# Performance work log

Measured on AMD Instinct MI355X. Metric: run time of the kernel, lower is better.

Reference implementation:

```python
import jax, jax.numpy as jnp
import numpy as np

LN_EPS = 1e-5

def _layernorm(x, g, b):
    mu = jnp.mean(x, axis=-1, keepdims=True)
    var = jnp.var(x, axis=-1, keepdims=True)
    return (x - mu) * jax.lax.rsqrt(var + LN_EPS) * g + b

def setup_inputs() -> dict:
    key = jax.random.key(0)
    ks = jax.random.split(key, 12)
    B, E, R = 32, 64, 36
    Dt, Di, D = 768, 2048, 512
    s = 0.02
    return {
        "text_feats": jax.random.normal(ks[0], (B, E, Dt), jnp.float32),
        "image_feats": jax.random.normal(ks[1], (B, R, Di), jnp.float32),
        "W_text": jax.random.normal(ks[2], (Dt, D), jnp.float32) * s,
        "b_text": jnp.zeros((D,), jnp.float32),
        "g_text": jnp.ones((D,), jnp.float32),
        "beta_text": jnp.zeros((D,), jnp.float32),
        "W_img": jax.random.normal(ks[3], (Di, D), jnp.float32) * s,
        "b_img": jnp.zeros((D,), jnp.float32),
        "g_img": jnp.ones((D,), jnp.float32),
        "beta_img": jnp.zeros((D,), jnp.float32),
        "W1": jax.random.normal(ks[4], (2 * D, D), jnp.float32) * s,
        "b1": jnp.zeros((D,), jnp.float32),
        "W2": jax.random.normal(ks[5], (D, 1), jnp.float32) * s,
        "b2": jnp.zeros((1,), jnp.float32),
    }

def reference(text_feats, image_feats, W_text, b_text, g_text, beta_text,
              W_img, b_img, g_img, beta_img, W1, b1, W2, b2):
    B, E, _ = text_feats.shape
    R = image_feats.shape[1]
    D = W_text.shape[1]
    # projections: Linear -> ReLU -> LayerNorm
    text_aligned = _layernorm(jax.nn.relu(text_feats @ W_text + b_text), g_text, beta_text)   # [B,E,D]
    image_aligned = _layernorm(jax.nn.relu(image_feats @ W_img + b_img), g_img, beta_img)     # [B,R,D]
    # pairwise scorer: split W1 to avoid materializing the [B,E,R,2D] concat
    W1_t, W1_i = W1[:D], W1[D:]
    h_t = text_aligned @ W1_t                 # [B,E,D]
    h_i = image_aligned @ W1_i + b1           # [B,R,D]
    h = jax.nn.relu(h_t[:, :, None, :] + h_i[:, None, :, :])  # [B,E,R,D]
    scores_raw = jnp.squeeze(h @ W2, -1) + b2[0]               # [B,E,R]
    alignment_scores = jax.nn.sigmoid(scores_raw)
    # softmax over flattened (E*R) per batch
    w = jax.nn.softmax(alignment_scores.reshape(B, E * R), axis=1).reshape(B, E, R)
    # weighted sum over regions, mean over entities
    aggregated = jnp.einsum('ber,brd->bd', w, image_aligned) / E   # [B,D]
    return alignment_scores, aggregated
```

## Files before the change

kernel.cpp:

```cpp
#include <hip/hip_runtime.h>
#include <math.h>

#define LN_EPS 1e-5f

typedef __attribute__((ext_vector_type(8))) short bf16x8;
typedef __attribute__((ext_vector_type(4))) float f32x4;
typedef unsigned short ushort_t;
typedef unsigned int uint_t;

__device__ __forceinline__ ushort_t f2bf(float f) {
    uint_t u = __float_as_uint(f);
    u += 0x7FFF + ((u >> 16) & 1);
    return (ushort_t)(u >> 16);
}

__global__ __launch_bounds__(256) void prep_kernel(
    const float* __restrict__ text, const float* __restrict__ image,
    ushort_t* __restrict__ text_bf, ushort_t* __restrict__ image_bf,
    const float* __restrict__ W_text, const float* __restrict__ W_img,
    const float* __restrict__ W1,
    ushort_t* __restrict__ Wt_t, ushort_t* __restrict__ Wi_t,
    ushort_t* __restrict__ W1t_t, ushort_t* __restrict__ W1i_t)
{
    __shared__ float t[32][33];
    const int bid = blockIdx.x;
    if (bid < 3840) {
        const int i4 = (bid * 256 + threadIdx.x) * 4;
        const float* src; ushort_t* dst; int off;
        if (i4 < 1572864) { src = text;  dst = text_bf;  off = i4; }
        else              { src = image; dst = image_bf; off = i4 - 1572864; }
        float4 v = *(const float4*)(src + off);
        ushort4 o;
        o.x = f2bf(v.x); o.y = f2bf(v.y); o.z = f2bf(v.z); o.w = f2bf(v.w);
        *(ushort4*)(dst + off) = o;
        return;
    }
    int local = bid - 3840;
    const float* src; ushort_t* dst; int K;
    if      (local < 384)  { src = W_text;         dst = Wt_t;  K = 768;  }
    else if (local < 1408) { src = W_img;          dst = Wi_t;  K = 2048; local -= 384; }
    else if (local < 1664) { src = W1;             dst = W1t_t; K = 512;  local -= 1408; }
    else                   { src = W1 + 512 * 512; dst = W1i_t; K = 512;  local -= 1664; }
    const int ntk = K / 32;
    const int k0 = (local % ntk) * 32;
    const int n0 = (local / ntk) * 32;
    const int x = threadIdx.x % 32, y = threadIdx.x / 32;
    #pragma unroll
    for (int j = 0; j < 4; ++j)
        t[y + 8 * j][x] = src[(size_t)(k0 + y + 8 * j) * 512 + n0 + x];
    __syncthreads();
    #pragma unroll
    for (int j = 0; j < 4; ++j)
        dst[(size_t)(n0 + y + 8 * j) * K + k0 + x] = f2bf(t[x][y + 8 * j]);
}

__global__ __launch_bounds__(256) void gemm_splitk_kernel(
    const ushort_t* __restrict__ A0, const ushort_t* __restrict__ B0,
    const float* __restrict__ bias0, float* __restrict__ C0, int K0,
    const ushort_t* __restrict__ A1, const ushort_t* __restrict__ B1,
    const float* __restrict__ bias1, float* __restrict__ C1, int K1,
    int ysplit, int relu)
{
    __shared__ float red[4][64][64];

    const ushort_t* A; const ushort_t* Bt; const float* bias; float* C; int K;
    int yy = blockIdx.y;
    if (yy < ysplit) { A = A0; Bt = B0; bias = bias0; C = C0; K = K0; }
    else { A = A1; Bt = B1; bias = bias1; C = C1; K = K1; yy -= ysplit; }

    const int tid  = threadIdx.x;
    const int wave = tid >> 6;
    const int lane = tid & 63;
    const int q    = lane >> 4;
    const int mj   = lane & 15;
    const int brow = yy * 64;
    const int bcol = blockIdx.x * 64;

    const ushort_t* Ab = A  + (size_t)(brow + mj) * K + q * 8;
    const ushort_t* Bb = Bt + (size_t)(bcol + mj) * K + q * 8;
    const int kw0    = wave * (K >> 2);
    const int ksteps = K >> 7;

    f32x4 acc[4][4] = {};

    #pragma unroll 2
    for (int s = 0; s < ksteps; ++s) {
        const int k = kw0 + s * 32;
        bf16x8 af[4], bf[4];
        #pragma unroll
        for (int i = 0; i < 4; ++i) {
            af[i] = *(const bf16x8*)(Ab + (size_t)i * 16 * K + k);
            bf[i] = *(const bf16x8*)(Bb + (size_t)i * 16 * K + k);
        }
        #pragma unroll
        for (int mi = 0; mi < 4; ++mi)
            #pragma unroll
            for (int ni = 0; ni < 4; ++ni)
                acc[mi][ni] = __builtin_amdgcn_mfma_f32_16x16x32_bf16(
                    af[mi], bf[ni], acc[mi][ni], 0, 0, 0);
    }

    #pragma unroll
    for (int mi = 0; mi < 4; ++mi)
        #pragma unroll
        for (int ni = 0; ni < 4; ++ni)
            #pragma unroll
            for (int r = 0; r < 4; ++r)
                red[wave][mi * 16 + q * 4 + r][ni * 16 + mj] = acc[mi][ni][r];
    __syncthreads();

    #pragma unroll
    for (int g = 0; g < 4; ++g) {
        const int idx = g * 1024 + tid * 4;
        const int row = idx >> 6, col = idx & 63;
        float4 v0 = *(float4*)&red[0][row][col];
        float4 v1 = *(float4*)&red[1][row][col];
        float4 v2 = *(float4*)&red[2][row][col];
        float4 v3 = *(float4*)&red[3][row][col];
        float4 o;
        o.x = (v0.x + v1.x) + (v2.x + v3.x);
        o.y = (v0.y + v1.y) + (v2.y + v3.y);
        o.z = (v0.z + v1.z) + (v2.z + v3.z);
        o.w = (v0.w + v1.w) + (v2.w + v3.w);
        if (bias) {
            float4 bv = *(const float4*)&bias[bcol + col];
            o.x += bv.x; o.y += bv.y; o.z += bv.z; o.w += bv.w;
        }
        if (relu) {
            o.x = fmaxf(o.x, 0.f); o.y = fmaxf(o.y, 0.f);
            o.z = fmaxf(o.z, 0.f); o.w = fmaxf(o.w, 0.f);
        }
        *(float4*)&C[(size_t)(brow + row) * 512 + bcol + col] = o;
    }
}

__global__ __launch_bounds__(256) void ln_fused_kernel(
    float* __restrict__ ta, const float* __restrict__ g_t,
    const float* __restrict__ be_t, ushort_t* __restrict__ ta_bf,
    float* __restrict__ ia, const float* __restrict__ g_i,
    const float* __restrict__ be_i, ushort_t* __restrict__ ia_bf)
{
    const int tid = threadIdx.x;
    int row = blockIdx.x;
    float* p; const float* g; const float* beta; ushort_t* obf; float* ofp;
    if (row < 2048) {
        p = ta + (size_t)row * 512; g = g_t; beta = be_t;
        obf = ta_bf + (size_t)row * 512; ofp = nullptr;
    } else {
        row -= 2048;
        p = ia + (size_t)row * 512; g = g_i; beta = be_i;
        obf = ia_bf + (size_t)row * 512; ofp = p;
    }

    float2 v = *(const float2*)&p[tid * 2];
    float s  = v.x + v.y;
    float ss = v.x * v.x + v.y * v.y;
    #pragma unroll
    for (int off = 32; off; off >>= 1) {
        s  += __shfl_down(s, off);
        ss += __shfl_down(ss, off);
    }
    __shared__ float red[8];
    if ((tid & 63) == 0) { red[(tid >> 6) * 2] = s; red[(tid >> 6) * 2 + 1] = ss; }
    __syncthreads();
    __shared__ float stats[2];
    if (tid == 0) {
        float S  = red[0] + red[2] + red[4] + red[6];
        float SS = red[1] + red[3] + red[5] + red[7];
        float mu  = S * (1.f / 512.f);
        float var = SS * (1.f / 512.f) - mu * mu;
        stats[0] = mu;
        stats[1] = rsqrtf(var + LN_EPS);
    }
    __syncthreads();
    const float mu = stats[0], rstd = stats[1];
    float2 gv = *(const float2*)&g[tid * 2];
    float2 bv = *(const float2*)&beta[tid * 2];
    float o0 = (v.x - mu) * rstd * gv.x + bv.x;
    float o1 = (v.y - mu) * rstd * gv.y + bv.y;
    ushort2 ob; ob.x = f2bf(o0); ob.y = f2bf(o1);
    *(ushort2*)&obf[tid * 2] = ob;
    if (ofp) {
        float2 of; of.x = o0; of.y = o1;
        *(float2*)&ofp[tid * 2] = of;
    }
}

__global__ __launch_bounds__(256) void scores_kernel(
    const float* __restrict__ ht, const float* __restrict__ hi,
    const float* __restrict__ W2, const float* __restrict__ b2,
    float* __restrict__ scores)
{
    const int be   = blockIdx.x;
    const int b    = be >> 6;
    const int tid  = threadIdx.x;
    const int lane = tid & 63;
    const int wave = tid >> 6;

    float htv[8], w2v[8];
    const float* htp = ht + (size_t)be * 512;
    #pragma unroll
    for (int j = 0; j < 8; ++j) {
        htv[j] = htp[lane + 64 * j];
        w2v[j] = W2[lane + 64 * j];
    }
    const float bb = b2[0];
    const float* hib = hi + (size_t)b * 36 * 512;

    for (int r = wave; r < 36; r += 4) {
        const float* hir = hib + (size_t)r * 512;
        float acc = 0.f;
        #pragma unroll
        for (int j = 0; j < 8; ++j) {
            float h = fmaxf(htv[j] + hir[lane + 64 * j], 0.f);
            acc = fmaf(h, w2v[j], acc);
        }
        #pragma unroll
        for (int off = 32; off; off >>= 1) acc += __shfl_down(acc, off);
        if (lane == 0) {
            float sr = acc + bb;
            scores[(size_t)be * 36 + r] = 1.f / (1.f + expf(-sr));
        }
    }
}

__global__ __launch_bounds__(256) void agg_kernel(
    const float* __restrict__ scores, const float* __restrict__ img,
    float* __restrict__ outAgg)
{
    const int b   = blockIdx.x;
    const int tid = threadIdx.x;
    const float* sc = scores + (size_t)b * 2304;

    __shared__ float part[4][36];
    __shared__ float sexp[36];
    __shared__ float inv_s;

    const int e4 = tid >> 6;
    const int r  = tid & 63;
    if (r < 36) {
        float p = 0.f;
        #pragma unroll
        for (int e = 0; e < 16; ++e) p += expf(sc[(e * 4 + e4) * 36 + r]);
        part[e4][r] = p;
    }
    __syncthreads();
    if (tid < 36) sexp[tid] = part[0][tid] + part[1][tid] + part[2][tid] + part[3][tid];
    __syncthreads();
    if (tid < 64) {
        float v = (tid < 36) ? sexp[tid] : 0.f;
        #pragma unroll
        for (int off = 32; off; off >>= 1) v += __shfl_down(v, off);
        if (tid == 0) inv_s = 1.f / (v * 64.f);
    }
    __syncthreads();
    const float inv = inv_s;

    const float* ib = img + (size_t)b * 36 * 512;
    for (int d = tid; d < 512; d += 256) {
        float acc = 0.f;
        #pragma unroll
        for (int rr = 0; rr < 36; ++rr)
            acc = fmaf(sexp[rr] * inv, ib[rr * 512 + d], acc);
        outAgg[(size_t)b * 512 + d] = acc;
    }
}

extern "C" void kernel_launch(void* const* d_in, const int* in_sizes, int n_in,
                              void* d_out, int out_size, void* d_ws, size_t ws_size,
                              hipStream_t stream)
{
    const float* text      = (const float*)d_in[0];
    const float* image     = (const float*)d_in[1];
    const float* W_text    = (const float*)d_in[2];
    const float* b_text    = (const float*)d_in[3];
    const float* g_text    = (const float*)d_in[4];
    const float* beta_text = (const float*)d_in[5];
    const float* W_img     = (const float*)d_in[6];
    const float* b_img     = (const float*)d_in[7];
    const float* g_img     = (const float*)d_in[8];
    const float* beta_img  = (const float*)d_in[9];
    const float* W1        = (const float*)d_in[10];
    const float* b1        = (const float*)d_in[11];
    const float* W2        = (const float*)d_in[12];
    const float* b2        = (const float*)d_in[13];

    float* out_scores = (float*)d_out;
    float* out_agg    = (float*)d_out + 73728;

    char* ws = (char*)d_ws;
    float*    ta       = (float*)(ws);
    float*    ia       = (float*)(ws + (4u << 20));
    ushort_t* text_bf  = (ushort_t*)(ws + 6402048);
    ushort_t* image_bf = (ushort_t*)(ws + 6402048 + 3145728);
    float*    ht       = (float*)(ws + 6402048);
    float*    hi       = (float*)(ws + 6402048 + 4194304);
    char*     wbase    = ws + 6402048 + 7864320;
    ushort_t* Wt_t     = (ushort_t*)(wbase);
    ushort_t* Wi_t     = (ushort_t*)(wbase + 786432);
    ushort_t* W1t_t    = (ushort_t*)(wbase + 786432 + 2097152);
    ushort_t* W1i_t    = (ushort_t*)(wbase + 786432 + 2097152 + 524288);
    char*     bfbase   = wbase + 786432 + 2097152 + 2 * 524288;
    ushort_t* ta_bf    = (ushort_t*)(bfbase);
    ushort_t* ia_bf    = (ushort_t*)(bfbase + 2097152);

    prep_kernel<<<5760, 256, 0, stream>>>(text, image, text_bf, image_bf,
                                          W_text, W_img, W1,
                                          Wt_t, Wi_t, W1t_t, W1i_t);
    gemm_splitk_kernel<<<dim3(8, 50), 256, 0, stream>>>(
        text_bf, Wt_t, b_text, ta, 768,
        image_bf, Wi_t, b_img, ia, 2048,
        32, 1);
    ln_fused_kernel<<<3200, 256, 0, stream>>>(ta, g_text, beta_text, ta_bf,
                                              ia, g_img, beta_img, ia_bf);
    gemm_splitk_kernel<<<dim3(8, 50), 256, 0, stream>>>(
        ta_bf, W1t_t, nullptr, ht, 512,
        ia_bf, W1i_t, b1, hi, 512,
        32, 0);
    scores_kernel<<<2048, 256, 0, stream>>>(ht, hi, W2, b2, out_scores);
    agg_kernel<<<32, 256, 0, stream>>>(out_scores, ia, out_agg);
}
```

Baseline: 150.2 us.

## Fuse all stages into one persistent kernel with software grid barriers

Replaces six kernel launches with a single persistent kernel of 1024 blocks that runs prep, projection GEMM, layernorm, second GEMM, scoring and aggregation. Stages are separated by hierarchical atomic grid barriers, which removes launch gaps and inter-kernel drain. It also changes the GEMM wave split from 4-way split-K to 2 K-halves by 2 N-halves, halving the reduction buffer, and splits aggregation across 64 blocks. The risks are barrier overhead, a deadlock if the 1024 blocks cannot all be resident at once, idle blocks during the 400-tile GEMM phases, and an extra memset launch.

```diff
diff --git a/kernel.cpp b/kernel.cpp
--- a/kernel.cpp
+++ b/kernel.cpp
@@ -2,6 +2,7 @@
 #include <math.h>
 
 #define LN_EPS 1e-5f
+#define NBLK 1024
 
 typedef __attribute__((ext_vector_type(8))) short bf16x8;
 typedef __attribute__((ext_vector_type(4))) float f32x4;
@@ -14,88 +15,66 @@
     return (ushort_t)(u >> 16);
 }
 
-__global__ __launch_bounds__(256) void prep_kernel(
-    const float* __restrict__ text, const float* __restrict__ image,
-    ushort_t* __restrict__ text_bf, ushort_t* __restrict__ image_bf,
-    const float* __restrict__ W_text, const float* __restrict__ W_img,
-    const float* __restrict__ W1,
-    ushort_t* __restrict__ Wt_t, ushort_t* __restrict__ Wi_t,
-    ushort_t* __restrict__ W1t_t, ushort_t* __restrict__ W1i_t)
+union SMU {
+    float red[2][64][64];
+    float tmat[32][33];
+    struct { float red8[8]; float stats[2]; } ln;
+    struct { float part[4][36]; float sexp[36]; float inv_s; } agg;
+};
+
+__device__ __forceinline__ void gbar(uint_t* cnt, int phase) {
+    __syncthreads();
+    if (threadIdx.x == 0) {
+        __threadfence();
+        uint_t* sub = cnt + (blockIdx.x & 15) * 32;
+        uint_t* mst = cnt + 512;
+        uint_t old = atomicAdd(sub, 1u);
+        if (old == (uint_t)(phase * (NBLK / 16) - 1))
+            atomicAdd(mst, 1u);
+        int it = 0;
+        while (__hip_atomic_load(mst, __ATOMIC_RELAXED, __HIP_MEMORY_SCOPE_AGENT)
+               < (uint_t)(phase * 16)) {
+            __builtin_amdgcn_s_sleep(4);
+            if (++it > (1 << 20)) break;
+        }
+        __threadfence();
+    }
+    __syncthreads();
+}
+
+__device__ __forceinline__ void do_gemm(
+    const ushort_t* __restrict__ A, const ushort_t* __restrict__ Bt,
+    const float* __restrict__ bias, float* __restrict__ C, int K,
+    int yy, int bx, int relu, float (&red)[2][64][64])
 {
-    __shared__ float t[32][33];
-    const int bid = blockIdx.x;
-    if (bid < 3840) {
-        const int i4 = (bid * 256 + threadIdx.x) * 4;
-        const float* src; ushort_t* dst; int off;
-        if (i4 < 1572864) { src = text;  dst = text_bf;  off = i4; }
-        else              { src = image; dst = image_bf; off = i4 - 1572864; }
-        float4 v = *(const float4*)(src + off);
-        ushort4 o;
-        o.x = f2bf(v.x); o.y = f2bf(v.y); o.z = f2bf(v.z); o.w = f2bf(v.w);
-        *(ushort4*)(dst + off) = o;
-        return;
-    }
-    int local = bid - 3840;
-    const float* src; ushort_t* dst; int K;
-    if      (local < 384)  { src = W_text;         dst = Wt_t;  K = 768;  }
-    else if (local < 1408) { src = W_img;          dst = Wi_t;  K = 2048; local -= 384; }
-    else if (local < 1664) { src = W1;             dst = W1t_t; K = 512;  local -= 1408; }
-    else                   { src = W1 + 512 * 512; dst = W1i_t; K = 512;  local -= 1664; }
-    const int ntk = K / 32;
-    const int k0 = (local % ntk) * 32;
-    const int n0 = (local / ntk) * 32;
-    const int x = threadIdx.x % 32, y = threadIdx.x / 32;
-    #pragma unroll
-    for (int j = 0; j < 4; ++j)
-        t[y + 8 * j][x] = src[(size_t)(k0 + y + 8 * j) * 512 + n0 + x];
-    __syncthreads();
-    #pragma unroll
-    for (int j = 0; j < 4; ++j)
-        dst[(size_t)(n0 + y + 8 * j) * K + k0 + x] = f2bf(t[x][y + 8 * j]);
-}
-
-__global__ __launch_bounds__(256) void gemm_splitk_kernel(
-    const ushort_t* __restrict__ A0, const ushort_t* __restrict__ B0,
-    const float* __restrict__ bias0, float* __restrict__ C0, int K0,
-    const ushort_t* __restrict__ A1, const ushort_t* __restrict__ B1,
-    const float* __restrict__ bias1, float* __restrict__ C1, int K1,
-    int ysplit, int relu)
-{
-    __shared__ float red[4][64][64];
-
-    const ushort_t* A; const ushort_t* Bt; const float* bias; float* C; int K;
-    int yy = blockIdx.y;
-    if (yy < ysplit) { A = A0; Bt = B0; bias = bias0; C = C0; K = K0; }
-    else { A = A1; Bt = B1; bias = bias1; C = C1; K = K1; yy -= ysplit; }
-
     const int tid  = threadIdx.x;
     const int wave = tid >> 6;
     const int lane = tid & 63;
+    const int kw   = wave >> 1;
+    const int nw   = wave & 1;
     const int q    = lane >> 4;
     const int mj   = lane & 15;
     const int brow = yy * 64;
-    const int bcol = blockIdx.x * 64;
-
-    const ushort_t* Ab = A  + (size_t)(brow + mj) * K + q * 8;
-    const ushort_t* Bb = Bt + (size_t)(bcol + mj) * K + q * 8;
-    const int kw0    = wave * (K >> 2);
-    const int ksteps = K >> 7;
-
-    f32x4 acc[4][4] = {};
-
+    const int bcol = bx * 64;
+
+    const ushort_t* Ab = A  + (size_t)(brow + mj) * K + kw * (K >> 1) + q * 8;
+    const ushort_t* Bb = Bt + (size_t)(bcol + nw * 32 + mj) * K + kw * (K >> 1) + q * 8;
+    const int ksteps = K >> 6;
+
+    f32x4 acc[4][2] = {};
     #pragma unroll 2
     for (int s = 0; s < ksteps; ++s) {
-        const int k = kw0 + s * 32;
-        bf16x8 af[4], bf[4];
-        #pragma unroll
-        for (int i = 0; i < 4; ++i) {
-            af[i] = *(const bf16x8*)(Ab + (size_t)i * 16 * K + k);
-            bf[i] = *(const bf16x8*)(Bb + (size_t)i * 16 * K + k);
-        }
+        bf16x8 af[4], bf[2];
+        #pragma unroll
+        for (int i = 0; i < 4; ++i)
+            af[i] = *(const bf16x8*)(Ab + (size_t)i * 16 * K + s * 32);
+        #pragma unroll
+        for (int i = 0; i < 2; ++i)
+            bf[i] = *(const bf16x8*)(Bb + (size_t)i * 16 * K + s * 32);
         #pragma unroll
         for (int mi = 0; mi < 4; ++mi)
             #pragma unroll
-            for (int ni = 0; ni < 4; ++ni)
+            for (int ni = 0; ni < 2; ++ni)
                 acc[mi][ni] = __builtin_amdgcn_mfma_f32_16x16x32_bf16(
                     af[mi], bf[ni], acc[mi][ni], 0, 0, 0);
     }
@@ -103,10 +82,10 @@
     #pragma unroll
     for (int mi = 0; mi < 4; ++mi)
         #pragma unroll
-        for (int ni = 0; ni < 4; ++ni)
+        for (int ni = 0; ni < 2; ++ni)
             #pragma unroll
             for (int r = 0; r < 4; ++r)
-                red[wave][mi * 16 + q * 4 + r][ni * 16 + mj] = acc[mi][ni][r];
+                red[kw][mi * 16 + q * 4 + r][nw * 32 + ni * 16 + mj] = acc[mi][ni][r];
     __syncthreads();
 
     #pragma unroll
@@ -115,13 +94,9 @@
         const int row = idx >> 6, col = idx & 63;
         float4 v0 = *(float4*)&red[0][row][col];
         float4 v1 = *(float4*)&red[1][row][col];
-        float4 v2 = *(float4*)&red[2][row][col];
-        float4 v3 = *(float4*)&red[3][row][col];
         float4 o;
-        o.x = (v0.x + v1.x) + (v2.x + v3.x);
-        o.y = (v0.y + v1.y) + (v2.y + v3.y);
-        o.z = (v0.z + v1.z) + (v2.z + v3.z);
-        o.w = (v0.w + v1.w) + (v2.w + v3.w);
+        o.x = v0.x + v1.x; o.y = v0.y + v1.y;
+        o.z = v0.z + v1.z; o.w = v0.w + v1.w;
         if (bias) {
             float4 bv = *(const float4*)&bias[bcol + col];
             o.x += bv.x; o.y += bv.y; o.z += bv.z; o.w += bv.w;
@@ -134,135 +109,186 @@
     }
 }
 
-__global__ __launch_bounds__(256) void ln_fused_kernel(
-    float* __restrict__ ta, const float* __restrict__ g_t,
-    const float* __restrict__ be_t, ushort_t* __restrict__ ta_bf,
-    float* __restrict__ ia, const float* __restrict__ g_i,
-    const float* __restrict__ be_i, ushort_t* __restrict__ ia_bf)
+__global__ __launch_bounds__(256, 4) void mega_kernel(
+    const float* __restrict__ text, const float* __restrict__ image,
+    const float* __restrict__ W_text, const float* __restrict__ b_text,
+    const float* __restrict__ g_text, const float* __restrict__ beta_text,
+    const float* __restrict__ W_img, const float* __restrict__ b_img,
+    const float* __restrict__ g_img, const float* __restrict__ beta_img,
+    const float* __restrict__ W1, const float* __restrict__ b1,
+    const float* __restrict__ W2, const float* __restrict__ b2,
+    float* __restrict__ out_scores, float* __restrict__ out_agg,
+    float* ta, float* ia, ushort_t* text_bf, ushort_t* image_bf,
+    float* ht, float* hi,
+    ushort_t* Wt_t, ushort_t* Wi_t, ushort_t* W1t_t, ushort_t* W1i_t,
+    ushort_t* ta_bf, ushort_t* ia_bf, uint_t* cnt)
 {
+    __shared__ SMU sm;
     const int tid = threadIdx.x;
-    int row = blockIdx.x;
-    float* p; const float* g; const float* beta; ushort_t* obf; float* ofp;
-    if (row < 2048) {
-        p = ta + (size_t)row * 512; g = g_t; beta = be_t;
-        obf = ta_bf + (size_t)row * 512; ofp = nullptr;
-    } else {
-        row -= 2048;
-        p = ia + (size_t)row * 512; g = g_i; beta = be_i;
-        obf = ia_bf + (size_t)row * 512; ofp = p;
-    }
-
-    float2 v = *(const float2*)&p[tid * 2];
-    float s  = v.x + v.y;
-    float ss = v.x * v.x + v.y * v.y;
-    #pragma unroll
-    for (int off = 32; off; off >>= 1) {
-        s  += __shfl_down(s, off);
-        ss += __shfl_down(ss, off);
-    }
-    __shared__ float red[8];
-    if ((tid & 63) == 0) { red[(tid >> 6) * 2] = s; red[(tid >> 6) * 2 + 1] = ss; }
-    __syncthreads();
-    __shared__ float stats[2];
-    if (tid == 0) {
-        float S  = red[0] + red[2] + red[4] + red[6];
-        float SS = red[1] + red[3] + red[5] + red[7];
-        float mu  = S * (1.f / 512.f);
-        float var = SS * (1.f / 512.f) - mu * mu;
-        stats[0] = mu;
-        stats[1] = rsqrtf(var + LN_EPS);
-    }
-    __syncthreads();
-    const float mu = stats[0], rstd = stats[1];
-    float2 gv = *(const float2*)&g[tid * 2];
-    float2 bv = *(const float2*)&beta[tid * 2];
-    float o0 = (v.x - mu) * rstd * gv.x + bv.x;
-    float o1 = (v.y - mu) * rstd * gv.y + bv.y;
-    ushort2 ob; ob.x = f2bf(o0); ob.y = f2bf(o1);
-    *(ushort2*)&obf[tid * 2] = ob;
-    if (ofp) {
-        float2 of; of.x = o0; of.y = o1;
-        *(float2*)&ofp[tid * 2] = of;
-    }
-}
-
-__global__ __launch_bounds__(256) void scores_kernel(
-    const float* __restrict__ ht, const float* __restrict__ hi,
-    const float* __restrict__ W2, const float* __restrict__ b2,
-    float* __restrict__ scores)
-{
-    const int be   = blockIdx.x;
-    const int b    = be >> 6;
-    const int tid  = threadIdx.x;
-    const int lane = tid & 63;
-    const int wave = tid >> 6;
-
-    float htv[8], w2v[8];
-    const float* htp = ht + (size_t)be * 512;
-    #pragma unroll
-    for (int j = 0; j < 8; ++j) {
-        htv[j] = htp[lane + 64 * j];
-        w2v[j] = W2[lane + 64 * j];
-    }
-    const float bb = b2[0];
-    const float* hib = hi + (size_t)b * 36 * 512;
-
-    for (int r = wave; r < 36; r += 4) {
-        const float* hir = hib + (size_t)r * 512;
+    const int bid = blockIdx.x;
+
+    for (int vb = bid; vb < 5760; vb += NBLK) {
+        if (vb < 3840) {
+            const int i4 = (vb * 256 + tid) * 4;
+            const float* src; ushort_t* dst; int off;
+            if (i4 < 1572864) { src = text;  dst = text_bf;  off = i4; }
+            else              { src = image; dst = image_bf; off = i4 - 1572864; }
+            float4 v = *(const float4*)(src + off);
+            ushort4 o;
+            o.x = f2bf(v.x); o.y = f2bf(v.y); o.z = f2bf(v.z); o.w = f2bf(v.w);
+            *(ushort4*)(dst + off) = o;
+        } else {
+            int local = vb - 3840;
+            const float* src; ushort_t* dst; int K;
+            if      (local < 384)  { src = W_text;       dst = Wt_t;  K = 768;  }
+            else if (local < 1408) { src = W_img;        dst = Wi_t;  K = 2048; local -= 384; }
+            else if (local < 1664) { src = W1;           dst = W1t_t; K = 512;  local -= 1408; }
+            else                   { src = W1 + 512*512; dst = W1i_t; K = 512;  local -= 1664; }
+            const int ntk = K / 32;
+            const int k0 = (local % ntk) * 32;
+            const int n0 = (local / ntk) * 32;
+            const int x = tid % 32, y = tid / 32;
+            #pragma unroll
+            for (int j = 0; j < 4; ++j)
+                sm.tmat[y + 8 * j][x] = src[(size_t)(k0 + y + 8 * j) * 512 + n0 + x];
+            __syncthreads();
+            #pragma unroll
+            for (int j = 0; j < 4; ++j)
+                dst[(size_t)(n0 + y + 8 * j) * K + k0 + x] = f2bf(sm.tmat[x][y + 8 * j]);
+            __syncthreads();
+        }
+    }
+    gbar(cnt, 1);
+
+    if (bid < 400) {
+        const int t  = (bid & 7) * 50 + (bid >> 3);
+        const int yy = t >> 3, x = t & 7;
+        if (yy < 32) do_gemm(text_bf,  Wt_t, b_text, ta, 768,  yy,      x, 1, sm.red);
+        else         do_gemm(image_bf, Wi_t, b_img,  ia, 2048, yy - 32, x, 1, sm.red);
+    }
+    gbar(cnt, 2);
+
+    for (int rr = bid; rr < 3200; rr += NBLK) {
+        int row = rr;
+        float* p; const float* g; const float* beta; ushort_t* obf; float* ofp;
+        if (row < 2048) {
+            p = ta + (size_t)row * 512; g = g_text; beta = beta_text;
+            obf = ta_bf + (size_t)row * 512; ofp = nullptr;
+        } else {
+            row -= 2048;
+            p = ia + (size_t)row * 512; g = g_img; beta = beta_img;
+            obf = ia_bf + (size_t)row * 512; ofp = ia + (size_t)row * 512;
+        }
+        float2 v = *(const float2*)&p[tid * 2];
+        float s  = v.x + v.y;
+        float ss = v.x * v.x + v.y * v.y;
+        #pragma unroll
+        for (int off = 32; off; off >>= 1) {
+            s  += __shfl_down(s, off);
+            ss += __shfl_down(ss, off);
+        }
+        if ((tid & 63) == 0) {
+            sm.ln.red8[(tid >> 6) * 2]     = s;
+            sm.ln.red8[(tid >> 6) * 2 + 1] = ss;
+        }
+        __syncthreads();
+        if (tid == 0) {
+            float S  = sm.ln.red8[0] + sm.ln.red8[2] + sm.ln.red8[4] + sm.ln.red8[6];
+            float SS = sm.ln.red8[1] + sm.ln.red8[3] + sm.ln.red8[5] + sm.ln.red8[7];
+            float mu  = S * (1.f / 512.f);
+            float var = SS * (1.f / 512.f) - mu * mu;
+            sm.ln.stats[0] = mu;
+            sm.ln.stats[1] = rsqrtf(var + LN_EPS);
+        }
+        __syncthreads();
+        const float mu = sm.ln.stats[0], rstd = sm.ln.stats[1];
+        float2 gv = *(const float2*)&g[tid * 2];
+        float2 bv = *(const float2*)&beta[tid * 2];
+        float o0 = (v.x - mu) * rstd * gv.x + bv.x;
+        float o1 = (v.y - mu) * rstd * gv.y + bv.y;
+        ushort2 ob; ob.x = f2bf(o0); ob.y = f2bf(o1);
+        *(ushort2*)&obf[tid * 2] = ob;
+        if (ofp) { float2 of; of.x = o0; of.y = o1; *(float2*)&ofp[tid * 2] = of; }
+        __syncthreads();
+    }
+    gbar(cnt, 3);
+
+    if (bid < 400) {
+        const int t  = (bid & 7) * 50 + (bid >> 3);
+        const int yy = t >> 3, x = t & 7;
+        if (yy < 32) do_gemm(ta_bf, W1t_t, nullptr, ht, 512, yy,      x, 0, sm.red);
+        else         do_gemm(ia_bf, W1i_t, b1,      hi, 512, yy - 32, x, 0, sm.red);
+    }
+    gbar(cnt, 4);
+
+    {
+        const int lane = tid & 63;
+        const int wave = tid >> 6;
+        float w2v[8];
+        #pragma unroll
+        for (int j = 0; j < 8; ++j) w2v[j] = W2[lane + 64 * j];
+        const float bb = b2[0];
+        const int sbe = ((bid & 7) << 7) + (bid >> 3);
+        #pragma unroll
+        for (int u = 0; u < 2; ++u) {
+            const int be = sbe + u * 1024;
+            const int b  = be >> 6;
+            float htv[8];
+            const float* htp = ht + (size_t)be * 512;
+            #pragma unroll
+            for (int j = 0; j < 8; ++j) htv[j] = htp[lane + 64 * j];
+            const float* hib = hi + (size_t)b * 36 * 512;
+            for (int r = wave; r < 36; r += 4) {
+                const float* hir = hib + (size_t)r * 512;
+                float acc = 0.f;
+                #pragma unroll
+                for (int j = 0; j < 8; ++j) {
+                    float h = fmaxf(htv[j] + hir[lane + 64 * j], 0.f);
+                    acc = fmaf(h, w2v[j], acc);
+                }
+                #pragma unroll
+                for (int off = 32; off; off >>= 1) acc += __shfl_down(acc, off);
+                if (lane == 0) {
+                    float sr = acc + bb;
+                    out_scores[(size_t)be * 36 + r] = 1.f / (1.f + expf(-sr));
+                }
+            }
+        }
+    }
+    gbar(cnt, 5);
+
+    if (bid < 64) {
+        const int b  = bid >> 1;
+        const int d0 = (bid & 1) << 8;
+        const float* sc = out_scores + (size_t)b * 2304;
+        const int e4 = tid >> 6;
+        const int r  = tid & 63;
+        if (r < 36) {
+            float p = 0.f;
+            #pragma unroll
+            for (int e = 0; e < 16; ++e) p += expf(sc[(e * 4 + e4) * 36 + r]);
+            sm.agg.part[e4][r] = p;
+        }
+        __syncthreads();
+        if (tid < 36)
+            sm.agg.sexp[tid] = sm.agg.part[0][tid] + sm.agg.part[1][tid]
+                             + sm.agg.part[2][tid] + sm.agg.part[3][tid];
+        __syncthreads();
+        if (tid < 64) {
+            float v = (tid < 36) ? sm.agg.sexp[tid] : 0.f;
+            #pragma unroll
+            for (int off = 32; off; off >>= 1) v += __shfl_down(v, off);
+            if (tid == 0) sm.agg.inv_s = 1.f / (v * 64.f);
+        }
+        __syncthreads();
+        const float inv = sm.agg.inv_s;
+        const float* ib = ia + (size_t)b * 36 * 512;
+        const int d = d0 + tid;
         float acc = 0.f;
         #pragma unroll
-        for (int j = 0; j < 8; ++j) {
-            float h = fmaxf(htv[j] + hir[lane + 64 * j], 0.f);
-            acc = fmaf(h, w2v[j], acc);
-        }
-        #pragma unroll
-        for (int off = 32; off; off >>= 1) acc += __shfl_down(acc, off);
-        if (lane == 0) {
-            float sr = acc + bb;
-            scores[(size_t)be * 36 + r] = 1.f / (1.f + expf(-sr));
-        }
-    }
-}
-
-__global__ __launch_bounds__(256) void agg_kernel(
-    const float* __restrict__ scores, const float* __restrict__ img,
-    float* __restrict__ outAgg)
-{
-    const int b   = blockIdx.x;
-    const int tid = threadIdx.x;
-    const float* sc = scores + (size_t)b * 2304;
-
-    __shared__ float part[4][36];
-    __shared__ float sexp[36];
-    __shared__ float inv_s;
-
-    const int e4 = tid >> 6;
-    const int r  = tid & 63;
-    if (r < 36) {
-        float p = 0.f;
-        #pragma unroll
-        for (int e = 0; e < 16; ++e) p += expf(sc[(e * 4 + e4) * 36 + r]);
-        part[e4][r] = p;
-    }
-    __syncthreads();
-    if (tid < 36) sexp[tid] = part[0][tid] + part[1][tid] + part[2][tid] + part[3][tid];
-    __syncthreads();
-    if (tid < 64) {
-        float v = (tid < 36) ? sexp[tid] : 0.f;
-        #pragma unroll
-        for (int off = 32; off; off >>= 1) v += __shfl_down(v, off);
-        if (tid == 0) inv_s = 1.f / (v * 64.f);
-    }
-    __syncthreads();
-    const float inv = inv_s;
-
-    const float* ib = img + (size_t)b * 36 * 512;
-    for (int d = tid; d < 512; d += 256) {
-        float acc = 0.f;
-        #pragma unroll
-        for (int rr = 0; rr < 36; ++rr)
-            acc = fmaf(sexp[rr] * inv, ib[rr * 512 + d], acc);
-        outAgg[(size_t)b * 512 + d] = acc;
+        for (int rr2 = 0; rr2 < 36; ++rr2)
+            acc = fmaf(sm.agg.sexp[rr2] * inv, ib[rr2 * 512 + d], acc);
+        out_agg[(size_t)b * 512 + d] = acc;
     }
 }
 
@@ -303,20 +329,13 @@
     char*     bfbase   = wbase + 786432 + 2097152 + 2 * 524288;
     ushort_t* ta_bf    = (ushort_t*)(bfbase);
     ushort_t* ia_bf    = (ushort_t*)(bfbase + 2097152);
-
-    prep_kernel<<<5760, 256, 0, stream>>>(text, image, text_bf, image_bf,
-                                          W_text, W_img, W1,
-                                          Wt_t, Wi_t, W1t_t, W1i_t);
-    gemm_splitk_kernel<<<dim3(8, 50), 256, 0, stream>>>(
-        text_bf, Wt_t, b_text, ta, 768,
-        image_bf, Wi_t, b_img, ia, 2048,
-        32, 1);
-    ln_fused_kernel<<<3200, 256, 0, stream>>>(ta, g_text, beta_text, ta_bf,
-                                              ia, g_img, beta_img, ia_bf);
-    gemm_splitk_kernel<<<dim3(8, 50), 256, 0, stream>>>(
-        ta_bf, W1t_t, nullptr, ht, 512,
-        ia_bf, W1i_t, b1, hi, 512,
-        32, 0);
-    scores_kernel<<<2048, 256, 0, stream>>>(ht, hi, W2, b2, out_scores);
-    agg_kernel<<<32, 256, 0, stream>>>(out_scores, ia, out_agg);
-}
+    uint_t*   cnt      = (uint_t*)(ws + 25165824);
+
+    (void)hipMemsetAsync(cnt, 0, 4096, stream);
+    mega_kernel<<<NBLK, 256, 0, stream>>>(
+        text, image, W_text, b_text, g_text, beta_text,
+        W_img, b_img, g_img, beta_img, W1, b1, W2, b2,
+        out_scores, out_agg,
+        ta, ia, text_bf, image_bf, ht, hi,
+        Wt_t, Wi_t, W1t_t, W1i_t, ta_bf, ia_bf, cnt);
+}
```

Result: slower. 367.5 us (+144.6%).

## Fold LayerNorm into GEMM epilogues via atomic row stats and folded weights

Applied to the files above, without the earlier changes.

Removes the standalone LayerNorm kernel. The first GEMM's epilogue emits bf16 pre-norm activations and accumulates per-row sum and sum-of-squares with atomics. The second GEMM applies mean and rstd algebraically, using gamma folded into W1 and precomputed gamma·W1 and beta·W1 vectors. The aggregation kernel likewise applies normalization through coefficients, which saves a kernel launch and a full read/write pass over the activations. In exchange it adds atomics, a stats-zeroing block in prep, and extra bf16 rounding on the un-normalized activations, which may cost accuracy.

```diff
diff --git a/kernel.cpp b/kernel.cpp
--- a/kernel.cpp
+++ b/kernel.cpp
@@ -19,13 +19,17 @@
     ushort_t* __restrict__ text_bf, ushort_t* __restrict__ image_bf,
     const float* __restrict__ W_text, const float* __restrict__ W_img,
     const float* __restrict__ W1,
+    const float* __restrict__ g_text, const float* __restrict__ beta_text,
+    const float* __restrict__ g_img, const float* __restrict__ beta_img,
     ushort_t* __restrict__ Wt_t, ushort_t* __restrict__ Wi_t,
-    ushort_t* __restrict__ W1t_t, ushort_t* __restrict__ W1i_t)
+    ushort_t* __restrict__ W1t_g, ushort_t* __restrict__ W1i_g,
+    float* __restrict__ stats, float* __restrict__ vparts)
 {
     __shared__ float t[32][33];
     const int bid = blockIdx.x;
+    const int tid = threadIdx.x;
     if (bid < 3840) {
-        const int i4 = (bid * 256 + threadIdx.x) * 4;
+        const int i4 = (bid * 256 + tid) * 4;
         const float* src; ushort_t* dst; int off;
         if (i4 < 1572864) { src = text;  dst = text_bf;  off = i4; }
         else              { src = image; dst = image_bf; off = i4 - 1572864; }
@@ -36,53 +40,67 @@
         return;
     }
     int local = bid - 3840;
-    const float* src; ushort_t* dst; int K;
-    if      (local < 384)  { src = W_text;         dst = Wt_t;  K = 768;  }
-    else if (local < 1408) { src = W_img;          dst = Wi_t;  K = 2048; local -= 384; }
-    else if (local < 1664) { src = W1;             dst = W1t_t; K = 512;  local -= 1408; }
-    else                   { src = W1 + 512 * 512; dst = W1i_t; K = 512;  local -= 1664; }
-    const int ntk = K / 32;
-    const int k0 = (local % ntk) * 32;
-    const int n0 = (local / ntk) * 32;
-    const int x = threadIdx.x % 32, y = threadIdx.x / 32;
-    #pragma unroll
-    for (int j = 0; j < 4; ++j)
-        t[y + 8 * j][x] = src[(size_t)(k0 + y + 8 * j) * 512 + n0 + x];
-    __syncthreads();
-    #pragma unroll
-    for (int j = 0; j < 4; ++j)
-        dst[(size_t)(n0 + y + 8 * j) * K + k0 + x] = f2bf(t[x][y + 8 * j]);
-}
-
-__global__ __launch_bounds__(256) void gemm_splitk_kernel(
-    const ushort_t* __restrict__ A0, const ushort_t* __restrict__ B0,
-    const float* __restrict__ bias0, float* __restrict__ C0, int K0,
-    const ushort_t* __restrict__ A1, const ushort_t* __restrict__ B1,
-    const float* __restrict__ bias1, float* __restrict__ C1, int K1,
-    int ysplit, int relu)
-{
-    __shared__ float red[4][64][64];
-
-    const ushort_t* A; const ushort_t* Bt; const float* bias; float* C; int K;
-    int yy = blockIdx.y;
-    if (yy < ysplit) { A = A0; Bt = B0; bias = bias0; C = C0; K = K0; }
-    else { A = A1; Bt = B1; bias = bias1; C = C1; K = K1; yy -= ysplit; }
-
-    const int tid  = threadIdx.x;
-    const int wave = tid >> 6;
-    const int lane = tid & 63;
-    const int q    = lane >> 4;
-    const int mj   = lane & 15;
-    const int brow = yy * 64;
-    const int bcol = blockIdx.x * 64;
-
+    if (local < 1920) {
+        const float* src; ushort_t* dst; int K; const float* gs = nullptr;
+        if      (local < 384)  { src = W_text;       dst = Wt_t;  K = 768;  }
+        else if (local < 1408) { src = W_img;        dst = Wi_t;  K = 2048; local -= 384; }
+        else if (local < 1664) { src = W1;           dst = W1t_g; K = 512;  local -= 1408; gs = g_text; }
+        else                   { src = W1 + 512*512; dst = W1i_g; K = 512;  local -= 1664; gs = g_img; }
+        const int ntk = K / 32;
+        const int k0 = (local % ntk) * 32;
+        const int n0 = (local / ntk) * 32;
+        const int x = tid % 32, y = tid / 32;
+        #pragma unroll
+        for (int j = 0; j < 4; ++j)
+            t[y + 8 * j][x] = src[(size_t)(k0 + y + 8 * j) * 512 + n0 + x];
+        __syncthreads();
+        const float gv = gs ? gs[k0 + x] : 1.f;
+        #pragma unroll
+        for (int j = 0; j < 4; ++j)
+            dst[(size_t)(n0 + y + 8 * j) * K + k0 + x] = f2bf(t[x][y + 8 * j] * gv);
+        return;
+    }
+    if (local == 1920) {
+        for (int i = tid; i < 6400; i += 256) stats[i] = 0.f;
+        return;
+    }
+    {
+        const int j    = local - 1921;
+        const int half = j >> 2;
+        const int jj   = j & 3;
+        const float* cg = half ? g_img : g_text;
+        const float* cb = half ? beta_img : beta_text;
+        const float* Wb = W1 + (size_t)(half * 512 + jj * 128) * 512;
+        const int n = tid;
+        float ag0 = 0.f, ab0 = 0.f, ag1 = 0.f, ab1 = 0.f;
+        #pragma unroll 4
+        for (int k = 0; k < 128; ++k) {
+            const float c1 = cg[jj * 128 + k];
+            const float c2 = cb[jj * 128 + k];
+            const float w0 = Wb[(size_t)k * 512 + n];
+            const float w1 = Wb[(size_t)k * 512 + n + 256];
+            ag0 = fmaf(c1, w0, ag0); ab0 = fmaf(c2, w0, ab0);
+            ag1 = fmaf(c1, w1, ag1); ab1 = fmaf(c2, w1, ab1);
+        }
+        float* vg = vparts + (size_t)(half * 2 + 0) * 2048 + jj * 512;
+        float* vb = vparts + (size_t)(half * 2 + 1) * 2048 + jj * 512;
+        vg[n] = ag0; vg[n + 256] = ag1;
+        vb[n] = ab0; vb[n + 256] = ab1;
+    }
+}
+
+__device__ __forceinline__ void gemm_core(
+    const ushort_t* __restrict__ A, const ushort_t* __restrict__ Bt, int K,
+    int brow, int bcol, int wave, int lane, float (&red)[4][64][64])
+{
+    const int q  = lane >> 4;
+    const int mj = lane & 15;
     const ushort_t* Ab = A  + (size_t)(brow + mj) * K + q * 8;
     const ushort_t* Bb = Bt + (size_t)(bcol + mj) * K + q * 8;
     const int kw0    = wave * (K >> 2);
     const int ksteps = K >> 7;
 
     f32x4 acc[4][4] = {};
-
     #pragma unroll 2
     for (int s = 0; s < ksteps; ++s) {
         const int k = kw0 + s * 32;
@@ -99,7 +117,6 @@
                 acc[mi][ni] = __builtin_amdgcn_mfma_f32_16x16x32_bf16(
                     af[mi], bf[ni], acc[mi][ni], 0, 0, 0);
     }
-
     #pragma unroll
     for (int mi = 0; mi < 4; ++mi)
         #pragma unroll
@@ -108,6 +125,28 @@
             for (int r = 0; r < 4; ++r)
                 red[wave][mi * 16 + q * 4 + r][ni * 16 + mj] = acc[mi][ni][r];
     __syncthreads();
+}
+
+__global__ __launch_bounds__(256) void gemm1_kernel(
+    const ushort_t* __restrict__ A0, const ushort_t* __restrict__ B0,
+    const float* __restrict__ bias0, ushort_t* __restrict__ Cb0,
+    float* __restrict__ Cf0, float* __restrict__ st0, int K0,
+    const ushort_t* __restrict__ A1, const ushort_t* __restrict__ B1,
+    const float* __restrict__ bias1, ushort_t* __restrict__ Cb1,
+    float* __restrict__ Cf1, float* __restrict__ st1, int K1,
+    int ysplit)
+{
+    __shared__ float red[4][64][64];
+    const ushort_t* A; const ushort_t* Bt; const float* bias;
+    ushort_t* Cb; float* Cf; float* st; int K;
+    int yy = blockIdx.y;
+    if (yy < ysplit) { A=A0; Bt=B0; bias=bias0; Cb=Cb0; Cf=Cf0; st=st0; K=K0; }
+    else { A=A1; Bt=B1; bias=bias1; Cb=Cb1; Cf=Cf1; st=st1; K=K1; yy -= ysplit; }
+
+    const int tid  = threadIdx.x;
+    const int brow = yy * 64;
+    const int bcol = blockIdx.x * 64;
+    gemm_core(A, Bt, K, brow, bcol, tid >> 6, tid & 63, red);
 
     #pragma unroll
     for (int g = 0; g < 4; ++g) {
@@ -122,67 +161,89 @@
         o.y = (v0.y + v1.y) + (v2.y + v3.y);
         o.z = (v0.z + v1.z) + (v2.z + v3.z);
         o.w = (v0.w + v1.w) + (v2.w + v3.w);
+        float4 bv = *(const float4*)&bias[bcol + col];
+        o.x = fmaxf(o.x + bv.x, 0.f); o.y = fmaxf(o.y + bv.y, 0.f);
+        o.z = fmaxf(o.z + bv.z, 0.f); o.w = fmaxf(o.w + bv.w, 0.f);
+        ushort4 ob;
+        ob.x = f2bf(o.x); ob.y = f2bf(o.y); ob.z = f2bf(o.z); ob.w = f2bf(o.w);
+        *(ushort4*)&Cb[(size_t)(brow + row) * 512 + bcol + col] = ob;
+        if (Cf) *(float4*)&Cf[(size_t)(brow + row) * 512 + bcol + col] = o;
+        float s1 = (o.x + o.y) + (o.z + o.w);
+        float s2 = fmaf(o.x, o.x, fmaf(o.y, o.y, fmaf(o.z, o.z, o.w * o.w)));
+        #pragma unroll
+        for (int off = 8; off; off >>= 1) {
+            s1 += __shfl_down(s1, off, 16);
+            s2 += __shfl_down(s2, off, 16);
+        }
+        if ((tid & 15) == 0) {
+            atomicAdd(&st[(size_t)(brow + row) * 2],     s1);
+            atomicAdd(&st[(size_t)(brow + row) * 2 + 1], s2);
+        }
+    }
+}
+
+__global__ __launch_bounds__(256) void gemm2_kernel(
+    const ushort_t* __restrict__ A0, const ushort_t* __restrict__ B0,
+    const float* __restrict__ bias0, float* __restrict__ C0,
+    const float* __restrict__ st0, const float* __restrict__ gW0,
+    const float* __restrict__ bW0, int K0,
+    const ushort_t* __restrict__ A1, const ushort_t* __restrict__ B1,
+    const float* __restrict__ bias1, float* __restrict__ C1,
+    const float* __restrict__ st1, const float* __restrict__ gW1,
+    const float* __restrict__ bW1, int K1,
+    int ysplit)
+{
+    __shared__ float red[4][64][64];
+    const ushort_t* A; const ushort_t* Bt; const float* bias; float* C;
+    const float* st; const float* gW; const float* bW; int K;
+    int yy = blockIdx.y;
+    if (yy < ysplit) { A=A0; Bt=B0; bias=bias0; C=C0; st=st0; gW=gW0; bW=bW0; K=K0; }
+    else { A=A1; Bt=B1; bias=bias1; C=C1; st=st1; gW=gW1; bW=bW1; K=K1; yy -= ysplit; }
+
+    const int tid  = threadIdx.x;
+    const int brow = yy * 64;
+    const int bcol = blockIdx.x * 64;
+    gemm_core(A, Bt, K, brow, bcol, tid >> 6, tid & 63, red);
+
+    #pragma unroll
+    for (int g = 0; g < 4; ++g) {
+        const int idx = g * 1024 + tid * 4;
+        const int row = idx >> 6, col = idx & 63;
+        float4 v0 = *(float4*)&red[0][row][col];
+        float4 v1 = *(float4*)&red[1][row][col];
+        float4 v2 = *(float4*)&red[2][row][col];
+        float4 v3 = *(float4*)&red[3][row][col];
+        float4 s;
+        s.x = (v0.x + v1.x) + (v2.x + v3.x);
+        s.y = (v0.y + v1.y) + (v2.y + v3.y);
+        s.z = (v0.z + v1.z) + (v2.z + v3.z);
+        s.w = (v0.w + v1.w) + (v2.w + v3.w);
+        const float st1v = st[(size_t)(brow + row) * 2];
+        const float st2v = st[(size_t)(brow + row) * 2 + 1];
+        const float mu   = st1v * (1.f / 512.f);
+        const float var  = st2v * (1.f / 512.f) - mu * mu;
+        const float rstd = rsqrtf(var + LN_EPS);
+        const int c = bcol + col;
+        float4 gw = *(const float4*)&gW[c];
+        float4 bw = *(const float4*)&bW[c];
+        #pragma unroll
+        for (int j = 1; j < 4; ++j) {
+            float4 gp = *(const float4*)&gW[j * 512 + c];
+            float4 bp = *(const float4*)&bW[j * 512 + c];
+            gw.x += gp.x; gw.y += gp.y; gw.z += gp.z; gw.w += gp.w;
+            bw.x += bp.x; bw.y += bp.y; bw.z += bp.z; bw.w += bp.w;
+        }
+        const float rm = rstd * mu;
+        float4 o;
+        o.x = fmaf(rstd, s.x, fmaf(-rm, gw.x, bw.x));
+        o.y = fmaf(rstd, s.y, fmaf(-rm, gw.y, bw.y));
+        o.z = fmaf(rstd, s.z, fmaf(-rm, gw.z, bw.z));
+        o.w = fmaf(rstd, s.w, fmaf(-rm, gw.w, bw.w));
         if (bias) {
-            float4 bv = *(const float4*)&bias[bcol + col];
-            o.x += bv.x; o.y += bv.y; o.z += bv.z; o.w += bv.w;
-        }
-        if (relu) {
-            o.x = fmaxf(o.x, 0.f); o.y = fmaxf(o.y, 0.f);
-            o.z = fmaxf(o.z, 0.f); o.w = fmaxf(o.w, 0.f);
-        }
-        *(float4*)&C[(size_t)(brow + row) * 512 + bcol + col] = o;
-    }
-}
-
-__global__ __launch_bounds__(256) void ln_fused_kernel(
-    float* __restrict__ ta, const float* __restrict__ g_t,
-    const float* __restrict__ be_t, ushort_t* __restrict__ ta_bf,
-    float* __restrict__ ia, const float* __restrict__ g_i,
-    const float* __restrict__ be_i, ushort_t* __restrict__ ia_bf)
-{
-    const int tid = threadIdx.x;
-    int row = blockIdx.x;
-    float* p; const float* g; const float* beta; ushort_t* obf; float* ofp;
-    if (row < 2048) {
-        p = ta + (size_t)row * 512; g = g_t; beta = be_t;
-        obf = ta_bf + (size_t)row * 512; ofp = nullptr;
-    } else {
-        row -= 2048;
-        p = ia + (size_t)row * 512; g = g_i; beta = be_i;
-        obf = ia_bf + (size_t)row * 512; ofp = p;
-    }
-
-    float2 v = *(const float2*)&p[tid * 2];
-    float s  = v.x + v.y;
-    float ss = v.x * v.x + v.y * v.y;
-    #pragma unroll
-    for (int off = 32; off; off >>= 1) {
-        s  += __shfl_down(s, off);
-        ss += __shfl_down(ss, off);
-    }
-    __shared__ float red[8];
-    if ((tid & 63) == 0) { red[(tid >> 6) * 2] = s; red[(tid >> 6) * 2 + 1] = ss; }
-    __syncthreads();
-    __shared__ float stats[2];
-    if (tid == 0) {
-        float S  = red[0] + red[2] + red[4] + red[6];
-        float SS = red[1] + red[3] + red[5] + red[7];
-        float mu  = S * (1.f / 512.f);
-        float var = SS * (1.f / 512.f) - mu * mu;
-        stats[0] = mu;
-        stats[1] = rsqrtf(var + LN_EPS);
-    }
-    __syncthreads();
-    const float mu = stats[0], rstd = stats[1];
-    float2 gv = *(const float2*)&g[tid * 2];
-    float2 bv = *(const float2*)&beta[tid * 2];
-    float o0 = (v.x - mu) * rstd * gv.x + bv.x;
-    float o1 = (v.y - mu) * rstd * gv.y + bv.y;
-    ushort2 ob; ob.x = f2bf(o0); ob.y = f2bf(o1);
-    *(ushort2*)&obf[tid * 2] = ob;
-    if (ofp) {
-        float2 of; of.x = o0; of.y = o1;
-        *(float2*)&ofp[tid * 2] = of;
+            float4 bb = *(const float4*)&bias[c];
+            o.x += bb.x; o.y += bb.y; o.z += bb.z; o.w += bb.w;
+        }
+        *(float4*)&C[(size_t)(brow + row) * 512 + c] = o;
     }
 }
 
@@ -226,7 +287,8 @@
 
 __global__ __launch_bounds__(256) void agg_kernel(
     const float* __restrict__ scores, const float* __restrict__ img,
-    float* __restrict__ outAgg)
+    const float* __restrict__ stats, const float* __restrict__ g_img,
+    const float* __restrict__ beta_img, float* __restrict__ outAgg)
 {
     const int b   = blockIdx.x;
     const int tid = threadIdx.x;
@@ -235,6 +297,7 @@
     __shared__ float part[4][36];
     __shared__ float sexp[36];
     __shared__ float inv_s;
+    __shared__ float coef[36], cmu[36];
 
     const int e4 = tid >> 6;
     const int r  = tid & 63;
@@ -255,14 +318,29 @@
     }
     __syncthreads();
     const float inv = inv_s;
+    if (tid < 36) {
+        const float s1 = stats[(size_t)(b * 36 + tid) * 2];
+        const float s2 = stats[(size_t)(b * 36 + tid) * 2 + 1];
+        const float mu   = s1 * (1.f / 512.f);
+        const float var  = s2 * (1.f / 512.f) - mu * mu;
+        const float rstd = rsqrtf(var + LN_EPS);
+        const float c = sexp[tid] * inv * rstd;
+        coef[tid] = c;
+        cmu[tid]  = c * mu;
+    }
+    __syncthreads();
+    float S1 = 0.f;
+    #pragma unroll
+    for (int rr = 0; rr < 36; ++rr) S1 += cmu[rr];
+    const float S0 = 1.f / 64.f;
 
     const float* ib = img + (size_t)b * 36 * 512;
     for (int d = tid; d < 512; d += 256) {
         float acc = 0.f;
         #pragma unroll
         for (int rr = 0; rr < 36; ++rr)
-            acc = fmaf(sexp[rr] * inv, ib[rr * 512 + d], acc);
-        outAgg[(size_t)b * 512 + d] = acc;
+            acc = fmaf(coef[rr], ib[rr * 512 + d], acc);
+        outAgg[(size_t)b * 512 + d] = fmaf(g_img[d], acc - S1, beta_img[d] * S0);
     }
 }
 
@@ -289,34 +367,33 @@
     float* out_agg    = (float*)d_out + 73728;
 
     char* ws = (char*)d_ws;
-    float*    ta       = (float*)(ws);
-    float*    ia       = (float*)(ws + (4u << 20));
-    ushort_t* text_bf  = (ushort_t*)(ws + 6402048);
-    ushort_t* image_bf = (ushort_t*)(ws + 6402048 + 3145728);
-    float*    ht       = (float*)(ws + 6402048);
-    float*    hi       = (float*)(ws + 6402048 + 4194304);
-    char*     wbase    = ws + 6402048 + 7864320;
-    ushort_t* Wt_t     = (ushort_t*)(wbase);
-    ushort_t* Wi_t     = (ushort_t*)(wbase + 786432);
-    ushort_t* W1t_t    = (ushort_t*)(wbase + 786432 + 2097152);
-    ushort_t* W1i_t    = (ushort_t*)(wbase + 786432 + 2097152 + 524288);
-    char*     bfbase   = wbase + 786432 + 2097152 + 2 * 524288;
-    ushort_t* ta_bf    = (ushort_t*)(bfbase);
-    ushort_t* ia_bf    = (ushort_t*)(bfbase + 2097152);
-
-    prep_kernel<<<5760, 256, 0, stream>>>(text, image, text_bf, image_bf,
-                                          W_text, W_img, W1,
-                                          Wt_t, Wi_t, W1t_t, W1i_t);
-    gemm_splitk_kernel<<<dim3(8, 50), 256, 0, stream>>>(
-        text_bf, Wt_t, b_text, ta, 768,
-        image_bf, Wi_t, b_img, ia, 2048,
-        32, 1);
-    ln_fused_kernel<<<3200, 256, 0, stream>>>(ta, g_text, beta_text, ta_bf,
-                                              ia, g_img, beta_img, ia_bf);
-    gemm_splitk_kernel<<<dim3(8, 50), 256, 0, stream>>>(
-        ta_bf, W1t_t, nullptr, ht, 512,
-        ia_bf, W1i_t, b1, hi, 512,
-        32, 0);
+    ushort_t* ta_bf    = (ushort_t*)(ws);
+    ushort_t* ia_bf    = (ushort_t*)(ws + 2097152);
+    float*    ia       = (float*)(ws + 3276800);
+    float*    ht       = (float*)(ws + 5636096);
+    float*    hi       = (float*)(ws + 9830400);
+    ushort_t* text_bf  = (ushort_t*)(ws + 12189696);
+    ushort_t* image_bf = (ushort_t*)(ws + 15335424);
+    ushort_t* Wt_t     = (ushort_t*)(ws + 20054016);
+    ushort_t* Wi_t     = (ushort_t*)(ws + 20840448);
+    ushort_t* W1t_g    = (ushort_t*)(ws + 22937600);
+    ushort_t* W1i_g    = (ushort_t*)(ws + 23461888);
+    float*    stats    = (float*)(ws + 23986176);
+    float*    vparts   = (float*)(ws + 24011776);
+
+    prep_kernel<<<5769, 256, 0, stream>>>(
+        text, image, text_bf, image_bf, W_text, W_img, W1,
+        g_text, beta_text, g_img, beta_img,
+        Wt_t, Wi_t, W1t_g, W1i_g, stats, vparts);
+    gemm1_kernel<<<dim3(8, 50), 256, 0, stream>>>(
+        text_bf, Wt_t, b_text, ta_bf, nullptr, stats, 768,
+        image_bf, Wi_t, b_img, ia_bf, ia, stats + 4096, 2048,
+        32);
+    gemm2_kernel<<<dim3(8, 50), 256, 0, stream>>>(
+        ta_bf, W1t_g, nullptr, ht, stats,        vparts,        vparts + 2048, 512,
+        ia_bf, W1i_g, b1,      hi, stats + 4096, vparts + 4096, vparts + 6144, 512,
+        32);
     scores_kernel<<<2048, 256, 0, stream>>>(ht, hi, W2, b2, out_scores);
-    agg_kernel<<<32, 256, 0, stream>>>(out_scores, ia, out_agg);
-}
+    agg_kernel<<<32, 256, 0, stream>>>(out_scores, ia, stats + 4096,
+                                       g_img, beta_img, out_agg);
+}
```

After: 154.1 us. +2.6%, slower.
